# Kernel optimization log

Hardware: AMD Instinct MI355X
Metric: run time of the kernel (lower is better)

## Reference

```python
import jax, jax.numpy as jnp
import numpy as np

SPARSITY = 5      # sparsity_level
DIAG_EPS = 1e-6   # max(epsilon, 1e-6) regularizer on gram_active
NORM_EPS = 1e-10  # epsilon used for atom normalization


def setup_inputs() -> dict:
    key = jax.random.key(0)
    kx, kd = jax.random.split(key)
    M, N, B = 64, 512, 65536
    X = jax.random.normal(kx, (M, B), dtype=jnp.float32)
    D = jax.random.normal(kd, (M, N), dtype=jnp.float32)
    # normalize_atoms=True: unit-L2 columns
    D = D / (jnp.linalg.norm(D, axis=0, keepdims=True) + NORM_EPS)
    return {"X": X, "D": D}


def reference(X, D):
    """Batched Orthogonal Matching Pursuit (KSVDDictionaryLearning.batch_omp).

    X: (M, B) signals, D: (M, N) column-normalized dictionary.
    Returns sparse coefficients (N, B) with SPARSITY nonzeros per column.
    """
    M, B = X.shape
    N = D.shape[1]
    gram = D.T @ D            # (N, N)
    dt_x_t = (D.T @ X).T      # (B, N)
    coeff = jnp.zeros((N, B), X.dtype)
    mask = jnp.zeros((N, B), dtype=bool)
    batch_idx = jnp.arange(B)
    selected = []
    for k in range(SPARSITY):  # fixed small unroll; active-set size grows k+1
        residual = X - D @ coeff                  # (M, B)
        corr = D.T @ residual                     # (N, B)
        corr = jnp.where(mask, 0.0, corr)
        idx = jnp.argmax(jnp.abs(corr), axis=0)   # (B,)
        selected.append(idx)
        mask = mask.at[idx, batch_idx].set(True)
        active = jnp.stack(selected, axis=1)      # (B, k+1)
        # gram restricted to active atoms: (B, k+1, k+1)
        gram_active = gram[active[:, :, None], active[:, None, :]]
        gram_active = gram_active + DIAG_EPS * jnp.eye(k + 1, dtype=gram.dtype)
        rhs = jnp.take_along_axis(dt_x_t, active, axis=1)          # (B, k+1)
        sol = jnp.linalg.solve(gram_active, rhs[..., None])[..., 0]  # (B, k+1)
        # rebuild coefficients: active covers every atom selected so far,
        # so scattering solutions into zeros matches the torch in-place writes
        coeff = jnp.zeros((N, B), X.dtype).at[active.T, batch_idx[None, :]].set(sol.T)
    return coeff
```

## Files before the change

kernel.cpp:

```cpp
#include <hip/hip_runtime.h>
#include <math.h>

#define NATOMS  512
#define MROWS   64
#define BATCH   65536
#define BT      4
#define NSPARSE 5
#define DEPSF   1e-6f

typedef float v2f __attribute__((ext_vector_type(2)));

__global__ void ksvd_prep(const float* __restrict__ D,
                          float* __restrict__ gram) {
  const int idx = blockIdx.x * 256 + threadIdx.x;
  const int i = idx >> 9;
  const int j = idx & (NATOMS - 1);
  double acc = 0.0;
#pragma unroll 8
  for (int m = 0; m < MROWS; ++m)
    acc += (double)D[m * NATOMS + i] * (double)D[m * NATOMS + j];
  gram[idx] = (float)acc;
}

__device__ __forceinline__ float wave_max_nonneg(float x) {
  int v = __builtin_bit_cast(int, x);
#define DPP_MAX_STEP(ctrl)                                                   \
  {                                                                          \
    const int t = __builtin_amdgcn_update_dpp(0, v, (ctrl), 0xf, 0xf, true); \
    v = __builtin_bit_cast(                                                  \
        int, fmaxf(__builtin_bit_cast(float, v), __builtin_bit_cast(float, t))); \
  }
  DPP_MAX_STEP(0x111)
  DPP_MAX_STEP(0x112)
  DPP_MAX_STEP(0x114)
  DPP_MAX_STEP(0x118)
  DPP_MAX_STEP(0x142)
  DPP_MAX_STEP(0x143)
#undef DPP_MAX_STEP
  return __builtin_bit_cast(float, __builtin_amdgcn_readlane(v, 63));
}

__device__ __forceinline__ float readlane_f(float v, int l) {
  return __builtin_bit_cast(float,
      __builtin_amdgcn_readlane(__builtin_bit_cast(int, v), l));
}

__global__ __launch_bounds__(256, 4) void ksvd_main(
    const float* __restrict__ X, const float* __restrict__ D,
    const float* __restrict__ gram, float* __restrict__ out) {
  __shared__ union {
    float4 xs4[MROWS][BT / 2];
    float  dtxT[BT][NATOMS];
  } sh;

  const int t    = threadIdx.x;
  const int lane = t & 63;
  const int wave = t >> 6;
  const int b0   = blockIdx.x * BT;

  if (t < MROWS * 2) {
    const int m = t >> 1, p = t & 1;
    const float x0 = X[(size_t)m * BATCH + b0 + 2 * p];
    const float x1 = X[(size_t)m * BATCH + b0 + 2 * p + 1];
    float4 v; v.x = x0; v.y = x0; v.z = x1; v.w = x1;
    sh.xs4[m][p] = v;
  }
  __syncthreads();

  const int a0 = wave * 128 + 2 * lane;
  v2f accA[BT], accB[BT];
#pragma unroll
  for (int c = 0; c < BT; ++c) {
    accA[c].x = 0.f; accA[c].y = 0.f;
    accB[c].x = 0.f; accB[c].y = 0.f;
  }

#pragma unroll 4
  for (int m = 0; m < MROWS; m += 2) {
    const v2f dA = *reinterpret_cast<const v2f*>(&D[m * NATOMS + a0]);
    const v2f dB = *reinterpret_cast<const v2f*>(&D[(m + 1) * NATOMS + a0]);
    const float4 xa0 = sh.xs4[m][0];
    const float4 xa1 = sh.xs4[m][1];
    const float4 xb0 = sh.xs4[m + 1][0];
    const float4 xb1 = sh.xs4[m + 1][1];
    v2f xv;
    xv.x = xa0.x; xv.y = xa0.y; accA[0] = __builtin_elementwise_fma(dA, xv, accA[0]);
    xv.x = xa0.z; xv.y = xa0.w; accA[1] = __builtin_elementwise_fma(dA, xv, accA[1]);
    xv.x = xa1.x; xv.y = xa1.y; accA[2] = __builtin_elementwise_fma(dA, xv, accA[2]);
    xv.x = xa1.z; xv.y = xa1.w; accA[3] = __builtin_elementwise_fma(dA, xv, accA[3]);
    xv.x = xb0.x; xv.y = xb0.y; accB[0] = __builtin_elementwise_fma(dB, xv, accB[0]);
    xv.x = xb0.z; xv.y = xb0.w; accB[1] = __builtin_elementwise_fma(dB, xv, accB[1]);
    xv.x = xb1.x; xv.y = xb1.y; accB[2] = __builtin_elementwise_fma(dB, xv, accB[2]);
    xv.x = xb1.z; xv.y = xb1.w; accB[3] = __builtin_elementwise_fma(dB, xv, accB[3]);
  }
  __syncthreads();

#pragma unroll
  for (int c = 0; c < BT; ++c) {
    const v2f s = accA[c] + accB[c];
    *reinterpret_cast<v2f*>(&sh.dtxT[c][a0]) = s;
  }
  __syncthreads();

  const int cglob = b0 + wave;
  float dtxr[8];
  {
    const float4 f0 = *reinterpret_cast<const float4*>(&sh.dtxT[wave][8 * lane]);
    const float4 f1 = *reinterpret_cast<const float4*>(&sh.dtxT[wave][8 * lane + 4]);
    dtxr[0] = f0.x; dtxr[1] = f0.y; dtxr[2] = f0.z; dtxr[3] = f0.w;
    dtxr[4] = f1.x; dtxr[5] = f1.y; dtxr[6] = f1.z; dtxr[7] = f1.w;
  }

  int   idxs[NSPARSE];
  float gc[NSPARSE - 1][8];
  float L[NSPARSE][NSPARSE];
  float inv_d[NSPARSE];
  float y[NSPARSE];
  float sol[NSPARSE];

#pragma unroll
  for (int k = 0; k < NSPARSE; ++k) {
    float bv   = -1.0f;
    int   bn   = 0;
    float bdtx = 0.0f;
#pragma unroll
    for (int jj = 0; jj < 8; ++jj) {
      float cv = dtxr[jj];
#pragma unroll
      for (int s = 0; s < k; ++s) cv -= sol[s] * gc[s][jj];
      const float av = fabsf(cv);
      if (av > bv) { bv = av; bn = 8 * lane + jj; bdtx = dtxr[jj]; }
    }
    const float wmax = wave_max_nonneg(bv);
    const unsigned long long own = __ballot(bv == wmax);
    const int owner = __ffsll((long long)own) - 1;
    int idx = __builtin_amdgcn_readlane(bn, owner);
    idx = __builtin_amdgcn_readfirstlane(idx);
    idxs[k] = idx;

    const float rhsk = readlane_f(bdtx, owner);

    if (k < NSPARSE - 1) {
      const float4 g0 = *reinterpret_cast<const float4*>(
          &gram[(size_t)idx * NATOMS + 8 * lane]);
      const float4 g1 = *reinterpret_cast<const float4*>(
          &gram[(size_t)idx * NATOMS + 8 * lane + 4]);
      gc[k][0] = g0.x; gc[k][1] = g0.y; gc[k][2] = g0.z; gc[k][3] = g0.w;
      gc[k][4] = g1.x; gc[k][5] = g1.y; gc[k][6] = g1.z; gc[k][7] = g1.w;
    }

    float arowf[NSPARSE];
#pragma unroll
    for (int j = 0; j < k; ++j)
      arowf[j] = gram[(size_t)idx * NATOMS + idxs[j]];
    const float gdiag = gram[(size_t)idx * NATOMS + idx];

    float ss = gdiag + DEPSF;
#pragma unroll
    for (int j = 0; j < k; ++j) {
      float w = arowf[j];
#pragma unroll
      for (int tt = 0; tt < j; ++tt) w -= L[k][tt] * L[j][tt];
      w *= inv_d[j];
      L[k][j] = w;
      ss -= w * w;
    }
    const float inv = rsqrtf(ss);
    L[k][k]  = ss * inv;
    inv_d[k] = inv;

    {
      float s2 = rhsk;
#pragma unroll
      for (int j = 0; j < k; ++j) s2 -= L[k][j] * y[j];
      y[k] = s2 * inv;
    }
#pragma unroll
    for (int i = k; i >= 0; --i) {
      float s2 = y[i];
#pragma unroll
      for (int j = i + 1; j <= k; ++j) s2 -= L[j][i] * sol[j];
      sol[i] = s2 * inv_d[i];
    }
  }

  if (lane == 0) {
#pragma unroll
    for (int s = 0; s < NSPARSE; ++s)
      out[(size_t)idxs[s] * BATCH + cglob] = sol[s];
  }
}

extern "C" void kernel_launch(void* const* d_in, const int* in_sizes, int n_in,
                              void* d_out, int out_size, void* d_ws,
                              size_t ws_size, hipStream_t stream) {
  (void)in_sizes; (void)n_in; (void)out_size; (void)ws_size;
  const float* X = (const float*)d_in[0];
  const float* D = (const float*)d_in[1];
  float* out = (float*)d_out;
  float* gram = (float*)d_ws;

  ksvd_prep<<<(NATOMS * NATOMS) / 256, 256, 0, stream>>>(D, gram);
  hipMemsetAsync(out, 0, (size_t)NATOMS * BATCH * sizeof(float), stream);
  ksvd_main<<<BATCH / BT, 256, 0, stream>>>(X, D, gram, out);
}
```

Measured before the change: 190.9 us.

## Split each batch column's OMP across two waves with LDS argmax exchange

Doubles the block to 512 threads so two waves share each batch column, each handling 256 atoms with 4 per lane instead of 8. The projection step now gives each thread one atom column, and X is loaded as a float4 per row. Each OMP iteration merges the two waves' argmax through shared memory behind a block-wide barrier. This aims to raise parallelism and cut per-lane register and serial work, at the cost of five extra __syncthreads and doing the small Cholesky solve redundantly in both waves.

```diff
diff --git a/kernel.cpp b/kernel.cpp
--- a/kernel.cpp
+++ b/kernel.cpp
@@ -7,8 +7,6 @@
 #define BT      4
 #define NSPARSE 5
 #define DEPSF   1e-6f
-
-typedef float v2f __attribute__((ext_vector_type(2)));
 
 __global__ void ksvd_prep(const float* __restrict__ D,
                           float* __restrict__ gram) {
@@ -45,74 +43,60 @@
       __builtin_amdgcn_readlane(__builtin_bit_cast(int, v), l));
 }
 
-__global__ __launch_bounds__(256, 4) void ksvd_main(
+__global__ __launch_bounds__(512, 2) void ksvd_main(
     const float* __restrict__ X, const float* __restrict__ D,
     const float* __restrict__ gram, float* __restrict__ out) {
   __shared__ union {
-    float4 xs4[MROWS][BT / 2];
+    float4 xs4[MROWS];
     float  dtxT[BT][NATOMS];
   } sh;
+  __shared__ float exv[BT][NSPARSE][2];
+  __shared__ int   exn[BT][NSPARSE][2];
+  __shared__ float exd[BT][NSPARSE][2];
 
   const int t    = threadIdx.x;
   const int lane = t & 63;
-  const int wave = t >> 6;
+  const int w    = t >> 6;
+  const int cw   = w >> 1;
+  const int h    = w & 1;
   const int b0   = blockIdx.x * BT;
 
-  if (t < MROWS * 2) {
-    const int m = t >> 1, p = t & 1;
-    const float x0 = X[(size_t)m * BATCH + b0 + 2 * p];
-    const float x1 = X[(size_t)m * BATCH + b0 + 2 * p + 1];
-    float4 v; v.x = x0; v.y = x0; v.z = x1; v.w = x1;
-    sh.xs4[m][p] = v;
-  }
+  if (t < MROWS)
+    sh.xs4[t] = *reinterpret_cast<const float4*>(&X[(size_t)t * BATCH + b0]);
   __syncthreads();
 
-  const int a0 = wave * 128 + 2 * lane;
-  v2f accA[BT], accB[BT];
+  const int aw = 64 * w + lane;
+  float accA[BT], accB[BT];
 #pragma unroll
-  for (int c = 0; c < BT; ++c) {
-    accA[c].x = 0.f; accA[c].y = 0.f;
-    accB[c].x = 0.f; accB[c].y = 0.f;
-  }
+  for (int c = 0; c < BT; ++c) { accA[c] = 0.f; accB[c] = 0.f; }
 
 #pragma unroll 4
   for (int m = 0; m < MROWS; m += 2) {
-    const v2f dA = *reinterpret_cast<const v2f*>(&D[m * NATOMS + a0]);
-    const v2f dB = *reinterpret_cast<const v2f*>(&D[(m + 1) * NATOMS + a0]);
-    const float4 xa0 = sh.xs4[m][0];
-    const float4 xa1 = sh.xs4[m][1];
-    const float4 xb0 = sh.xs4[m + 1][0];
-    const float4 xb1 = sh.xs4[m + 1][1];
-    v2f xv;
-    xv.x = xa0.x; xv.y = xa0.y; accA[0] = __builtin_elementwise_fma(dA, xv, accA[0]);
-    xv.x = xa0.z; xv.y = xa0.w; accA[1] = __builtin_elementwise_fma(dA, xv, accA[1]);
-    xv.x = xa1.x; xv.y = xa1.y; accA[2] = __builtin_elementwise_fma(dA, xv, accA[2]);
-    xv.x = xa1.z; xv.y = xa1.w; accA[3] = __builtin_elementwise_fma(dA, xv, accA[3]);
-    xv.x = xb0.x; xv.y = xb0.y; accB[0] = __builtin_elementwise_fma(dB, xv, accB[0]);
-    xv.x = xb0.z; xv.y = xb0.w; accB[1] = __builtin_elementwise_fma(dB, xv, accB[1]);
-    xv.x = xb1.x; xv.y = xb1.y; accB[2] = __builtin_elementwise_fma(dB, xv, accB[2]);
-    xv.x = xb1.z; xv.y = xb1.w; accB[3] = __builtin_elementwise_fma(dB, xv, accB[3]);
+    const float dA = D[m * NATOMS + aw];
+    const float dB = D[(m + 1) * NATOMS + aw];
+    const float4 xa = sh.xs4[m];
+    const float4 xb = sh.xs4[m + 1];
+    accA[0] = fmaf(dA, xa.x, accA[0]); accB[0] = fmaf(dB, xb.x, accB[0]);
+    accA[1] = fmaf(dA, xa.y, accA[1]); accB[1] = fmaf(dB, xb.y, accB[1]);
+    accA[2] = fmaf(dA, xa.z, accA[2]); accB[2] = fmaf(dB, xb.z, accB[2]);
+    accA[3] = fmaf(dA, xa.w, accA[3]); accB[3] = fmaf(dB, xb.w, accB[3]);
   }
   __syncthreads();
-
 #pragma unroll
-  for (int c = 0; c < BT; ++c) {
-    const v2f s = accA[c] + accB[c];
-    *reinterpret_cast<v2f*>(&sh.dtxT[c][a0]) = s;
-  }
+  for (int c = 0; c < BT; ++c)
+    sh.dtxT[c][aw] = accA[c] + accB[c];
   __syncthreads();
 
-  const int cglob = b0 + wave;
-  float dtxr[8];
+  const int cglob = b0 + cw;
+  float dtxr[4];
   {
-    const float4 f0 = *reinterpret_cast<const float4*>(&sh.dtxT[wave][8 * lane]);
-    const float4 f1 = *reinterpret_cast<const float4*>(&sh.dtxT[wave][8 * lane + 4]);
-    dtxr[0] = f0.x; dtxr[1] = f0.y; dtxr[2] = f0.z; dtxr[3] = f0.w;
-    dtxr[4] = f1.x; dtxr[5] = f1.y; dtxr[6] = f1.z; dtxr[7] = f1.w;
+    const float4 f =
+        *reinterpret_cast<const float4*>(&sh.dtxT[cw][256 * h + 4 * lane]);
+    dtxr[0] = f.x; dtxr[1] = f.y; dtxr[2] = f.z; dtxr[3] = f.w;
   }
 
   int   idxs[NSPARSE];
-  float gc[NSPARSE - 1][8];
+  float gc[NSPARSE - 1][4];
   float L[NSPARSE][NSPARSE];
   float inv_d[NSPARSE];
   float y[NSPARSE];
@@ -124,29 +108,35 @@
     int   bn   = 0;
     float bdtx = 0.0f;
 #pragma unroll
-    for (int jj = 0; jj < 8; ++jj) {
+    for (int jj = 0; jj < 4; ++jj) {
       float cv = dtxr[jj];
 #pragma unroll
       for (int s = 0; s < k; ++s) cv -= sol[s] * gc[s][jj];
       const float av = fabsf(cv);
-      if (av > bv) { bv = av; bn = 8 * lane + jj; bdtx = dtxr[jj]; }
+      if (av > bv) { bv = av; bn = 256 * h + 4 * lane + jj; bdtx = dtxr[jj]; }
     }
     const float wmax = wave_max_nonneg(bv);
     const unsigned long long own = __ballot(bv == wmax);
     const int owner = __ffsll((long long)own) - 1;
-    int idx = __builtin_amdgcn_readlane(bn, owner);
+    int   widx = __builtin_amdgcn_readlane(bn, owner);
+    float wdtx = readlane_f(bdtx, owner);
+    widx = __builtin_amdgcn_readfirstlane(widx);
+
+    if (lane == 0) {
+      exv[cw][k][h] = wmax; exn[cw][k][h] = widx; exd[cw][k][h] = wdtx;
+    }
+    __syncthreads();
+    const float v0 = exv[cw][k][0], v1 = exv[cw][k][1];
+    const bool take0 = (v0 >= v1);
+    int idx = take0 ? exn[cw][k][0] : exn[cw][k][1];
+    const float rhsk = take0 ? exd[cw][k][0] : exd[cw][k][1];
     idx = __builtin_amdgcn_readfirstlane(idx);
     idxs[k] = idx;
 
-    const float rhsk = readlane_f(bdtx, owner);
-
     if (k < NSPARSE - 1) {
-      const float4 g0 = *reinterpret_cast<const float4*>(
-          &gram[(size_t)idx * NATOMS + 8 * lane]);
-      const float4 g1 = *reinterpret_cast<const float4*>(
-          &gram[(size_t)idx * NATOMS + 8 * lane + 4]);
-      gc[k][0] = g0.x; gc[k][1] = g0.y; gc[k][2] = g0.z; gc[k][3] = g0.w;
-      gc[k][4] = g1.x; gc[k][5] = g1.y; gc[k][6] = g1.z; gc[k][7] = g1.w;
+      const float4 g = *reinterpret_cast<const float4*>(
+          &gram[(size_t)idx * NATOMS + 256 * h + 4 * lane]);
+      gc[k][0] = g.x; gc[k][1] = g.y; gc[k][2] = g.z; gc[k][3] = g.w;
     }
 
     float arowf[NSPARSE];
@@ -158,12 +148,12 @@
     float ss = gdiag + DEPSF;
 #pragma unroll
     for (int j = 0; j < k; ++j) {
-      float w = arowf[j];
+      float ww = arowf[j];
 #pragma unroll
-      for (int tt = 0; tt < j; ++tt) w -= L[k][tt] * L[j][tt];
-      w *= inv_d[j];
-      L[k][j] = w;
-      ss -= w * w;
+      for (int tt = 0; tt < j; ++tt) ww -= L[k][tt] * L[j][tt];
+      ww *= inv_d[j];
+      L[k][j] = ww;
+      ss -= ww * ww;
     }
     const float inv = rsqrtf(ss);
     L[k][k]  = ss * inv;
@@ -184,7 +174,7 @@
     }
   }
 
-  if (lane == 0) {
+  if (h == 0 && lane == 0) {
 #pragma unroll
     for (int s = 0; s < NSPARSE; ++s)
       out[(size_t)idxs[s] * BATCH + cglob] = sol[s];
@@ -202,5 +192,5 @@
 
   ksvd_prep<<<(NATOMS * NATOMS) / 256, 256, 0, stream>>>(D, gram);
   hipMemsetAsync(out, 0, (size_t)NATOMS * BATCH * sizeof(float), stream);
-  ksvd_main<<<BATCH / BT, 256, 0, stream>>>(X, D, gram, out);
+  ksvd_main<<<BATCH / BT, 512, 0, stream>>>(X, D, gram, out);
 }
```

New measurement: 191.3 us. About the same (+0.2%).
